# Performance work log

Measured on AMD Instinct MI355X. Metric: run time of the kernel, lower is better.

## Reference

```python
import jax, jax.numpy as jnp
import numpy as np

N = 100_000
E = 1_600_000
F_IN = 128
HID = 64
HEADS = 2
HC = HID // HEADS  # 32 per-head channels
EPS = 1e-5
NEG_SLOPE = 0.2


def _layer_norm(x, g, b):
    mu = jnp.mean(x, axis=-1, keepdims=True)
    var = jnp.mean(jnp.square(x - mu), axis=-1, keepdims=True)
    return (x - mu) * jax.lax.rsqrt(var + EPS) * g + b


def _batch_norm(x, g, b):
    # training-mode batch statistics over the node axis (biased variance)
    mu = jnp.mean(x, axis=0, keepdims=True)
    var = jnp.mean(jnp.square(x - mu), axis=0, keepdims=True)
    return (x - mu) * jax.lax.rsqrt(var + EPS) * g + b


def _gcn_conv(x, src, dst, W, bias, n):
    # PyG GCNConv: self-loops already included in (src, dst); symmetric norm
    deg = jax.ops.segment_sum(jnp.ones_like(src, dtype=x.dtype), dst, num_segments=n)
    dinv = jnp.where(deg > 0, jax.lax.rsqrt(deg), 0.0)
    norm = dinv[src] * dinv[dst]                      # [E2]
    xw = x @ W                                        # [N, out]
    msg = xw[src] * norm[:, None]                     # gather + scale
    out = jax.ops.segment_sum(msg, dst, num_segments=n)
    return out + bias


def _gat_conv(x, src, dst, W, att_src, att_dst, bias, n):
    # PyG GATConv, heads=HEADS, concat=True (self-loops included in src/dst)
    xw = (x @ W).reshape(n, HEADS, HC)                # [N, H, C]
    a_s = jnp.sum(xw * att_src, axis=-1)              # [N, H]
    a_d = jnp.sum(xw * att_dst, axis=-1)              # [N, H]
    e = jax.nn.leaky_relu(a_s[src] + a_d[dst], NEG_SLOPE)  # [E2, H]
    m = jax.ops.segment_max(e, dst, num_segments=n)   # per-target max for stability
    e = jnp.exp(e - m[dst])
    denom = jax.ops.segment_sum(e, dst, num_segments=n)
    alpha = e / (denom[dst] + 1e-16)                  # neighborhood softmax
    out = jax.ops.segment_sum(xw[src] * alpha[:, :, None], dst, num_segments=n)
    return out.reshape(n, HEADS * HC) + bias


def setup_inputs() -> dict:
    key = jax.random.key(0)
    ks = jax.random.split(key, 20)
    f32 = jnp.float32
    d = {}
    d["accessibility_features"] = jax.random.normal(ks[0], (N, F_IN), dtype=f32)
    d["edge_index"] = jax.random.randint(ks[1], (2, E), 0, N, dtype=jnp.int64)
    # LayerNorm
    d["ln_g"] = jnp.ones((F_IN,), f32); d["ln_b"] = jnp.zeros((F_IN,), f32)
    # feature encoder
    d["enc_w1"] = jax.random.normal(ks[2], (F_IN, HID), f32) * (2.0 / (F_IN + HID)) ** 0.5
    d["enc_b1"] = jnp.zeros((HID,), f32)
    d["enc_w2"] = jax.random.normal(ks[3], (HID, HID), f32) * (1.0 / HID) ** 0.5
    d["enc_b2"] = jnp.zeros((HID,), f32)
    # GCN 1
    d["gcn1_w"] = jax.random.normal(ks[4], (HID, HID), f32) * (1.0 / HID) ** 0.5
    d["gcn1_b"] = jnp.zeros((HID,), f32)
    d["bn1_g"] = jnp.ones((HID,), f32); d["bn1_b"] = jnp.zeros((HID,), f32)
    # GAT
    d["gat_w"] = jax.random.normal(ks[5], (HID, HEADS * HC), f32) * (1.0 / HID) ** 0.5
    d["gat_as"] = jax.random.normal(ks[6], (HEADS, HC), f32) * 0.1
    d["gat_ad"] = jax.random.normal(ks[7], (HEADS, HC), f32) * 0.1
    d["gat_b"] = jnp.zeros((HEADS * HC,), f32)
    d["bn2_g"] = jnp.ones((HID,), f32); d["bn2_b"] = jnp.zeros((HID,), f32)
    # GCN 2 -> hidden//2
    d["gcn2_w"] = jax.random.normal(ks[8], (HID, HID // 2), f32) * (2.0 / (HID + HID // 2)) ** 0.5
    d["gcn2_b"] = jnp.zeros((HID // 2,), f32)
    d["bn3_g"] = jnp.ones((HID // 2,), f32); d["bn3_b"] = jnp.zeros((HID // 2,), f32)
    # prediction head
    d["pred_w1"] = jax.random.normal(ks[9], (HID // 2, HID // 4), f32) * (2.0 / (HID // 2 + HID // 4)) ** 0.5
    d["pred_b1"] = jnp.zeros((HID // 4,), f32)
    d["pred_w2"] = jax.random.normal(ks[10], (HID // 4, 1), f32) * (2.0 / (HID // 4 + 1)) ** 0.5
    d["pred_b2"] = jnp.zeros((1,), f32)
    return d


def reference(accessibility_features, edge_index, ln_g, ln_b, enc_w1, enc_b1,
              enc_w2, enc_b2, gcn1_w, gcn1_b, bn1_g, bn1_b, gat_w, gat_as,
              gat_ad, gat_b, bn2_g, bn2_b, gcn2_w, gcn2_b, bn3_g, bn3_b,
              pred_w1, pred_b1, pred_w2, pred_b2):
    n = accessibility_features.shape[0]
    loops = jnp.arange(n, dtype=edge_index.dtype)
    src = jnp.concatenate([edge_index[0], loops])   # add self-loops once
    dst = jnp.concatenate([edge_index[1], loops])

    x = _layer_norm(accessibility_features, ln_g, ln_b)
    x = jax.nn.relu(x @ enc_w1 + enc_b1)            # dropout = identity (eval)
    x = jax.nn.relu(x @ enc_w2 + enc_b2)

    x = _gcn_conv(x, src, dst, gcn1_w, gcn1_b, n)
    x = jax.nn.relu(_batch_norm(x, bn1_g, bn1_b))

    xa = _gat_conv(x, src, dst, gat_w, gat_as, gat_ad, gat_b, n)
    xa = jax.nn.relu(_batch_norm(xa, bn2_g, bn2_b))

    x = _gcn_conv(xa, src, dst, gcn2_w, gcn2_b, n)
    x = jax.nn.relu(_batch_norm(x, bn3_g, bn3_b))

    h = jax.nn.relu(x @ pred_w1 + pred_b1)
    svi = jax.nn.sigmoid((h @ pred_w2 + pred_b2).squeeze(-1))
    return svi
```

## Files before the change

kernel.cpp:

```cpp
#include <hip/hip_runtime.h>
#include <math.h>

#define F_IN 128
#define HID  64
#define EPS  1e-5f
#define NSLOPE 0.2f
#define BSH 9
#define MAXBUK 1024
#define EPB 4096
#define SPB 4096

__device__ __forceinline__ float lrelu(float x) { return x > 0.f ? x : NSLOPE * x; }


__global__ __launch_bounds__(256) void k_buk_count(const int* __restrict__ ei,
                                                   int* __restrict__ bukcnt, int E, int nbuk) {
  __shared__ int lc[MAXBUK];
  for (int k = threadIdx.x; k < nbuk; k += 256) lc[k] = 0;
  __syncthreads();
  int base = blockIdx.x * EPB, end = min(E, base + EPB);
  for (int t = base + threadIdx.x; t < end; t += 256) atomicAdd(&lc[ei[E + t] >> BSH], 1);
  __syncthreads();
  for (int k = threadIdx.x; k < nbuk; k += 256)
    if (lc[k]) atomicAdd(&bukcnt[k], lc[k]);
}

__global__ void k_buk_scan(const int* __restrict__ bukcnt, int* __restrict__ bukbase, int nbuk) {
  __shared__ int l[MAXBUK + 1];
  for (int k = threadIdx.x; k < nbuk; k += blockDim.x) l[k] = bukcnt[k];
  __syncthreads();
  if (threadIdx.x == 0) {
    int r = 0;
    for (int k = 0; k < nbuk; ++k) { int t = l[k]; l[k] = r; r += t; }
    l[nbuk] = r;
  }
  __syncthreads();
  for (int k = threadIdx.x; k <= nbuk; k += blockDim.x) bukbase[k] = l[k];
}

__global__ __launch_bounds__(256) void k_buk_scatter(const int* __restrict__ ei,
                                                     const int* __restrict__ bukbase,
                                                     int* __restrict__ bukcur,
                                                     int2* __restrict__ pairs, int E, int nbuk) {
  __shared__ int lc[MAXBUK];
  __shared__ int lbase[MAXBUK];
  for (int k = threadIdx.x; k < nbuk; k += 256) lc[k] = 0;
  __syncthreads();
  int base = blockIdx.x * EPB, end = min(E, base + EPB);
  for (int t = base + threadIdx.x; t < end; t += 256) atomicAdd(&lc[ei[E + t] >> BSH], 1);
  __syncthreads();
  for (int k = threadIdx.x; k < nbuk; k += 256) {
    int c = lc[k];
    lbase[k] = c ? atomicAdd(&bukcur[k], c) : 0;
  }
  __syncthreads();
  for (int k = threadIdx.x; k < nbuk; k += 256) lc[k] = 0;
  __syncthreads();
  for (int t = base + threadIdx.x; t < end; t += 256) {
    int s = ei[t], d = ei[E + t];
    int b = d >> BSH;
    int o = atomicAdd(&lc[b], 1);
    pairs[bukbase[b] + lbase[b] + o] = make_int2(s, d);
  }
}

__global__ __launch_bounds__(256) void k_buk_deg(const int2* __restrict__ pairs,
                                                 const int* __restrict__ bukbase,
                                                 int* __restrict__ ideg, int N) {
  __shared__ int ldeg[1 << BSH];
  int b = blockIdx.x;
  for (int k = threadIdx.x; k < (1 << BSH); k += 256) ldeg[k] = 0;
  __syncthreads();
  int s0 = bukbase[b], s1 = bukbase[b + 1], nb = b << BSH;
  for (int t = s0 + threadIdx.x; t < s1; t += 256) atomicAdd(&ldeg[pairs[t].y - nb], 1);
  __syncthreads();
  for (int k = threadIdx.x; k < (1 << BSH); k += 256) {
    int node = nb + k;
    if (node < N) ideg[node] = ldeg[k];
  }
}

__global__ __launch_bounds__(256) void k_scan_sums(const int* __restrict__ ideg,
                                                   int* __restrict__ bsum, int N) {
  __shared__ int red[256];
  int base = blockIdx.x * SPB + threadIdx.x * 16;
  int s = 0;
#pragma unroll
  for (int j = 0; j < 16; ++j) { int i = base + j; if (i < N) s += ideg[i] + 1; }
  red[threadIdx.x] = s;
  __syncthreads();
  for (int o = 128; o; o >>= 1) {
    if (threadIdx.x < o) red[threadIdx.x] += red[threadIdx.x + o];
    __syncthreads();
  }
  if (threadIdx.x == 0) bsum[blockIdx.x] = red[0];
}

__global__ void k_scan_tops(int* __restrict__ bsum, int nb) {
  __shared__ int l[MAXBUK];
  for (int k = threadIdx.x; k < nb; k += blockDim.x) l[k] = bsum[k];
  __syncthreads();
  if (threadIdx.x == 0) {
    int r = 0;
    for (int k = 0; k < nb; ++k) { int t = l[k]; l[k] = r; r += t; }
  }
  __syncthreads();
  for (int k = threadIdx.x; k < nb; k += blockDim.x) bsum[k] = l[k];
}

__global__ __launch_bounds__(256) void k_scan_apply(const int* __restrict__ ideg,
                                                    const int* __restrict__ bsum,
                                                    int* __restrict__ rowstart,
                                                    float* __restrict__ dinv,
                                                    int* __restrict__ csr, int N) {
  __shared__ int pre[256];
  int base = blockIdx.x * SPB + threadIdx.x * 16;
  int deg[16];
  int s = 0;
#pragma unroll
  for (int j = 0; j < 16; ++j) {
    int i = base + j;
    int d = (i < N) ? ideg[i] + 1 : 0;
    deg[j] = d; s += d;
  }
  pre[threadIdx.x] = s;
  __syncthreads();
  for (int o = 1; o < 256; o <<= 1) {
    int v = (threadIdx.x >= o) ? pre[threadIdx.x - o] : 0;
    __syncthreads();
    pre[threadIdx.x] += v;
    __syncthreads();
  }
  int off = bsum[blockIdx.x] + pre[threadIdx.x] - s;
#pragma unroll
  for (int j = 0; j < 16; ++j) {
    int i = base + j;
    if (i < N) {
      rowstart[i] = off;
      dinv[i] = rsqrtf((float)deg[j]);
      csr[off] = i;
      off += deg[j];
    }
  }
}

__global__ __launch_bounds__(256) void k_buk_fill(const int2* __restrict__ pairs,
                                                  const int* __restrict__ bukbase,
                                                  const int* __restrict__ rowstart,
                                                  int* __restrict__ csr) {
  __shared__ int lcur[1 << BSH];
  int b = blockIdx.x;
  for (int k = threadIdx.x; k < (1 << BSH); k += 256) lcur[k] = 0;
  __syncthreads();
  int s0 = bukbase[b], s1 = bukbase[b + 1], nb = b << BSH;
  for (int t = s0 + threadIdx.x; t < s1; t += 256) {
    int2 pr = pairs[t];
    int o = atomicAdd(&lcur[pr.y - nb], 1);
    csr[rowstart[pr.y] + 1 + o] = pr.x;
  }
}

__global__ void k_precomp(const float* __restrict__ w1, const float* __restrict__ ln_g,
                          const float* __restrict__ ln_b, const float* __restrict__ b1,
                          float* __restrict__ w1g, float* __restrict__ c1,
                          float* __restrict__ cb) {
  int j = threadIdx.x;
  float c1v = 0.f, cbv = 0.f;
  for (int k = 0; k < F_IN; ++k) {
    float w = w1[k * HID + j];
    float wg = ln_g[k] * w;
    w1g[k * HID + j] = wg;
    c1v += wg;
    cbv += ln_b[k] * w;
  }
  c1[j] = c1v;
  cb[j] = cbv + b1[j];
}

__global__ __launch_bounds__(256) void k_enc_fused(
    const float* __restrict__ x, const float* __restrict__ w1g,
    const float* __restrict__ c1, const float* __restrict__ cb,
    const float* __restrict__ w2, const float* __restrict__ b2,
    const float* __restrict__ w3, float* __restrict__ xw, int N) {
  int i = blockIdx.x * 256 + threadIdx.x;
  if (i >= N) return;
  const float4* xr = (const float4*)(x + (size_t)i * F_IN);
  float a[HID];
#pragma unroll
  for (int j = 0; j < HID; ++j) a[j] = 0.f;
  float s = 0.f, q = 0.f;
#pragma unroll 1
  for (int c = 0; c < F_IN / 4; ++c) {
    float4 xv = xr[c];
    s += xv.x + xv.y + xv.z + xv.w;
    q += xv.x * xv.x + xv.y * xv.y + xv.z * xv.z + xv.w * xv.w;
    const float* wr = w1g + c * 4 * HID;
#pragma unroll
    for (int e = 0; e < 4; ++e) {
      float xe = (e == 0) ? xv.x : (e == 1) ? xv.y : (e == 2) ? xv.z : xv.w;
      const float4* w4 = (const float4*)(wr + e * HID);
#pragma unroll
      for (int j4 = 0; j4 < HID / 4; ++j4) {
        float4 wv = w4[j4];
        a[j4 * 4 + 0] += xe * wv.x;
        a[j4 * 4 + 1] += xe * wv.y;
        a[j4 * 4 + 2] += xe * wv.z;
        a[j4 * 4 + 3] += xe * wv.w;
      }
    }
  }
  float mu = s * (1.f / F_IN);
  float var = q * (1.f / F_IN) - mu * mu;
  float rs = rsqrtf(var + EPS);
#pragma unroll
  for (int j = 0; j < HID; ++j)
    a[j] = fmaxf(rs * (a[j] - mu * c1[j]) + cb[j], 0.f);
  float b[HID];
#pragma unroll
  for (int j = 0; j < HID; ++j) b[j] = b2[j];
#pragma unroll
  for (int k = 0; k < HID; ++k) {
    float hk = a[k];
    const float4* w4 = (const float4*)(w2 + k * HID);
#pragma unroll
    for (int c4 = 0; c4 < HID / 4; ++c4) {
      float4 wv = w4[c4];
      b[c4 * 4 + 0] += hk * wv.x;
      b[c4 * 4 + 1] += hk * wv.y;
      b[c4 * 4 + 2] += hk * wv.z;
      b[c4 * 4 + 3] += hk * wv.w;
    }
  }
#pragma unroll
  for (int j = 0; j < HID; ++j) b[j] = fmaxf(b[j], 0.f);
#pragma unroll
  for (int j = 0; j < HID; ++j) a[j] = 0.f;
#pragma unroll
  for (int k = 0; k < HID; ++k) {
    float hk = b[k];
    const float4* w4 = (const float4*)(w3 + k * HID);
#pragma unroll
    for (int c4 = 0; c4 < HID / 4; ++c4) {
      float4 wv = w4[c4];
      a[c4 * 4 + 0] += hk * wv.x;
      a[c4 * 4 + 1] += hk * wv.y;
      a[c4 * 4 + 2] += hk * wv.z;
      a[c4 * 4 + 3] += hk * wv.w;
    }
  }
  float4* o4 = (float4*)(xw + (size_t)i * HID);
#pragma unroll
  for (int c4 = 0; c4 < HID / 4; ++c4)
    o4[c4] = make_float4(a[c4 * 4 + 0], a[c4 * 4 + 1], a[c4 * 4 + 2], a[c4 * 4 + 3]);
}

template <int FOUT, bool GAT, bool BNIN>
__global__ __launch_bounds__(256) void k_gemm_reg(
    const float* __restrict__ x, const float* __restrict__ w,
    const float* __restrict__ stats,
    const float* __restrict__ atts, const float* __restrict__ atd,
    float* __restrict__ out, float* __restrict__ a_s, float* __restrict__ a_d, int N) {
  int i = blockIdx.x * 256 + threadIdx.x;
  if (i >= N) return;
  const float4* xr = (const float4*)(x + (size_t)i * HID);
  float acc[FOUT];
#pragma unroll
  for (int j = 0; j < FOUT; ++j) acc[j] = 0.f;
#pragma unroll 1
  for (int c = 0; c < HID / 4; ++c) {
    float4 xv = xr[c];
    if (BNIN) {
      xv.x = fmaxf(xv.x * stats[c * 4 + 0] + stats[HID + c * 4 + 0], 0.f);
      xv.y = fmaxf(xv.y * stats[c * 4 + 1] + stats[HID + c * 4 + 1], 0.f);
      xv.z = fmaxf(xv.z * stats[c * 4 + 2] + stats[HID + c * 4 + 2], 0.f);
      xv.w = fmaxf(xv.w * stats[c * 4 + 3] + stats[HID + c * 4 + 3], 0.f);
    }
    const float* wr = w + c * 4 * FOUT;
#pragma unroll
    for (int e = 0; e < 4; ++e) {
      float xe = (e == 0) ? xv.x : (e == 1) ? xv.y : (e == 2) ? xv.z : xv.w;
      const float4* w4 = (const float4*)(wr + e * FOUT);
#pragma unroll
      for (int j4 = 0; j4 < FOUT / 4; ++j4) {
        float4 wv = w4[j4];
        acc[j4 * 4 + 0] += xe * wv.x;
        acc[j4 * 4 + 1] += xe * wv.y;
        acc[j4 * 4 + 2] += xe * wv.z;
        acc[j4 * 4 + 3] += xe * wv.w;
      }
    }
  }
  float4* o4 = (float4*)(out + (size_t)i * FOUT);
#pragma unroll
  for (int c4 = 0; c4 < FOUT / 4; ++c4)
    o4[c4] = make_float4(acc[c4 * 4 + 0], acc[c4 * 4 + 1], acc[c4 * 4 + 2], acc[c4 * 4 + 3]);
  if (GAT) {
    float s0 = 0.f, s1 = 0.f, d0 = 0.f, d1 = 0.f;
#pragma unroll
    for (int c = 0; c < 32; ++c) { s0 += acc[c] * atts[c]; d0 += acc[c] * atd[c]; }
#pragma unroll
    for (int c = 32; c < 64; ++c) { s1 += acc[c] * atts[c]; d1 += acc[c] * atd[c]; }
    a_s[i * 2] = s0; a_s[i * 2 + 1] = s1;
    a_d[i * 2] = d0; a_d[i * 2 + 1] = d1;
  }
}

__global__ __launch_bounds__(256) void k_gcn_pull64(
    const int* __restrict__ csr, const int* __restrict__ rowstart, const int* __restrict__ ideg,
    const float* __restrict__ dinv, const float* __restrict__ xw,
    float* __restrict__ out, int N) {
  int wave = threadIdx.x >> 6, lane = threadIdx.x & 63;
  int i = blockIdx.x * 4 + wave;
  if (i >= N) return;
  int row = rowstart[i], dg = ideg[i] + 1;
  float did = dinv[i];
  float acc = 0.f;
  for (int base = 0; base < dg; base += 64) {
    int cnt = min(64, dg - base);
    int sid = (lane < cnt) ? csr[row + base + lane] : 0;
    int n = 0;
    for (; n + 4 <= cnt; n += 4) {
      int s0 = __shfl(sid, n), s1 = __shfl(sid, n + 1);
      int s2 = __shfl(sid, n + 2), s3 = __shfl(sid, n + 3);
      acc += dinv[s0] * did * xw[s0 * 64 + lane] + dinv[s1] * did * xw[s1 * 64 + lane] +
             dinv[s2] * did * xw[s2 * 64 + lane] + dinv[s3] * did * xw[s3 * 64 + lane];
    }
    for (; n < cnt; ++n) {
      int s0 = __shfl(sid, n);
      acc += dinv[s0] * did * xw[s0 * 64 + lane];
    }
  }
  out[i * 64 + lane] = acc;
}

__global__ __launch_bounds__(256) void k_gcn_pull32(
    const int* __restrict__ csr, const int* __restrict__ rowstart, const int* __restrict__ ideg,
    const float* __restrict__ dinv, const float* __restrict__ xw,
    float* __restrict__ out, int N) {
  int wave = threadIdx.x >> 6, lane = threadIdx.x & 63;
  int half = lane >> 5, lf = lane & 31;
  int i = (blockIdx.x * 4 + wave) * 2 + half;
  if (i >= N) return;
  int row = rowstart[i], dg = ideg[i] + 1;
  float did = dinv[i];
  float acc = 0.f;
  for (int base = 0; base < dg; base += 32) {
    int cnt = min(32, dg - base);
    int sid = (lf < cnt) ? csr[row + base + lf] : 0;
    int n = 0;
    for (; n + 2 <= cnt; n += 2) {
      int s0 = __shfl(sid, n, 32), s1 = __shfl(sid, n + 1, 32);
      acc += dinv[s0] * did * xw[s0 * 32 + lf] + dinv[s1] * did * xw[s1 * 32 + lf];
    }
    for (; n < cnt; ++n) {
      int s0 = __shfl(sid, n, 32);
      acc += dinv[s0] * did * xw[s0 * 32 + lf];
    }
  }
  out[i * 32 + lf] = acc;
}

__global__ __launch_bounds__(256) void k_gat_attn(
    const int* __restrict__ csr, const int* __restrict__ rowstart, const int* __restrict__ ideg,
    const float* __restrict__ a_s, const float* __restrict__ a_d,
    float* __restrict__ m_, float* __restrict__ rden, int N) {
  int wave = threadIdx.x >> 6, lane = threadIdx.x & 63;
  int i = blockIdx.x * 4 + wave;
  if (i >= N) return;
  int row = rowstart[i], dg = ideg[i] + 1;
  float ad0 = a_d[i * 2], ad1 = a_d[i * 2 + 1];
  if (dg <= 64) {
    float e0 = -1e30f, e1 = -1e30f;
    if (lane < dg) {
      int s = csr[row + lane];
      e0 = lrelu(a_s[s * 2] + ad0);
      e1 = lrelu(a_s[s * 2 + 1] + ad1);
    }
    float m0 = e0, m1 = e1;
#pragma unroll
    for (int o = 32; o; o >>= 1) { m0 = fmaxf(m0, __shfl_xor(m0, o)); m1 = fmaxf(m1, __shfl_xor(m1, o)); }
    float s0 = (lane < dg) ? __expf(e0 - m0) : 0.f;
    float s1 = (lane < dg) ? __expf(e1 - m1) : 0.f;
#pragma unroll
    for (int o = 32; o; o >>= 1) { s0 += __shfl_xor(s0, o); s1 += __shfl_xor(s1, o); }
    if (lane == 0) {
      m_[i * 2] = m0; m_[i * 2 + 1] = m1;
      rden[i * 2] = 1.f / (s0 + 1e-16f); rden[i * 2 + 1] = 1.f / (s1 + 1e-16f);
    }
  } else {
    float m0 = -1e30f, m1 = -1e30f;
    for (int base = 0; base < dg; base += 64)
      if (base + lane < dg) {
        int s = csr[row + base + lane];
        m0 = fmaxf(m0, lrelu(a_s[s * 2] + ad0));
        m1 = fmaxf(m1, lrelu(a_s[s * 2 + 1] + ad1));
      }
#pragma unroll
    for (int o = 32; o; o >>= 1) { m0 = fmaxf(m0, __shfl_xor(m0, o)); m1 = fmaxf(m1, __shfl_xor(m1, o)); }
    float s0 = 0.f, s1 = 0.f;
    for (int base = 0; base < dg; base += 64)
      if (base + lane < dg) {
        int s = csr[row + base + lane];
        s0 += __expf(lrelu(a_s[s * 2] + ad0) - m0);
        s1 += __expf(lrelu(a_s[s * 2 + 1] + ad1) - m1);
      }
#pragma unroll
    for (int o = 32; o; o >>= 1) { s0 += __shfl_xor(s0, o); s1 += __shfl_xor(s1, o); }
    if (lane == 0) {
      m_[i * 2] = m0; m_[i * 2 + 1] = m1;
      rden[i * 2] = 1.f / (s0 + 1e-16f); rden[i * 2 + 1] = 1.f / (s1 + 1e-16f);
    }
  }
}

__global__ __launch_bounds__(256) void k_gat_pv(
    const int* __restrict__ csr, const int* __restrict__ rowstart, const int* __restrict__ ideg,
    const float* __restrict__ a_s, const float* __restrict__ a_d,
    const float* __restrict__ m_, const float* __restrict__ rden,
    const float* __restrict__ xw, float* __restrict__ out, int N) {
  int wave = threadIdx.x >> 6, lane = threadIdx.x & 63;
  int i = blockIdx.x * 4 + wave;
  if (i >= N) return;
  int row = rowstart[i], dg = ideg[i] + 1;
  int h = lane >> 5;
  float adh = a_d[i * 2 + h], mh = m_[i * 2 + h], rh = rden[i * 2 + h];
  float acc = 0.f;
  for (int base = 0; base < dg; base += 64) {
    int cnt = min(64, dg - base);
    int sid = (lane < cnt) ? csr[row + base + lane] : 0;
    int n = 0;
    for (; n + 2 <= cnt; n += 2) {
      int s0 = __shfl(sid, n), s1 = __shfl(sid, n + 1);
      float al0 = __expf(lrelu(a_s[s0 * 2 + h] + adh) - mh) * rh;
      float al1 = __expf(lrelu(a_s[s1 * 2 + h] + adh) - mh) * rh;
      acc += al0 * xw[s0 * HID + lane] + al1 * xw[s1 * HID + lane];
    }
    for (; n < cnt; ++n) {
      int s0 = __shfl(sid, n);
      float al0 = __expf(lrelu(a_s[s0 * 2 + h] + adh) - mh) * rh;
      acc += al0 * xw[s0 * HID + lane];
    }
  }
  out[i * HID + lane] = acc;
}

template <int F>
__global__ __launch_bounds__(256) void k_bn_reduce(const float* __restrict__ x,
                                                   float* __restrict__ partials, int N) {
  __shared__ float sS[F], sQ[F];
  int tid = threadIdx.x;
  int t = blockIdx.x * 256 + tid;
  int stride = gridDim.x * 256;
  int total4 = N * F / 4;
  int f0 = (t * 4) % F;
  float s0 = 0, s1 = 0, s2 = 0, s3 = 0, q0 = 0, q1 = 0, q2 = 0, q3 = 0;
  for (int c = t; c < total4; c += stride) {
    float4 v = ((const float4*)x)[c];
    s0 += v.x; q0 += v.x * v.x;
    s1 += v.y; q1 += v.y * v.y;
    s2 += v.z; q2 += v.z * v.z;
    s3 += v.w; q3 += v.w * v.w;
  }
  if (tid < F) { sS[tid] = 0.f; sQ[tid] = 0.f; }
  __syncthreads();
  atomicAdd(&sS[f0], s0);     atomicAdd(&sQ[f0], q0);
  atomicAdd(&sS[f0 + 1], s1); atomicAdd(&sQ[f0 + 1], q1);
  atomicAdd(&sS[f0 + 2], s2); atomicAdd(&sQ[f0 + 2], q2);
  atomicAdd(&sS[f0 + 3], s3); atomicAdd(&sQ[f0 + 3], q3);
  __syncthreads();
  if (tid < F) {
    partials[blockIdx.x * 2 * F + tid]     = sS[tid];
    partials[blockIdx.x * 2 * F + F + tid] = sQ[tid];
  }
}

template <int F>
__global__ void k_bn_finalize(const float* __restrict__ partials, int nblk,
                              float* __restrict__ stats, const float* __restrict__ g,
                              const float* __restrict__ b, int N) {
  int f = threadIdx.x;
  if (f >= F) return;
  float s = 0.f, q = 0.f;
  for (int k = 0; k < nblk; ++k) {
    s += partials[k * 2 * F + f];
    q += partials[k * 2 * F + F + f];
  }
  float mu = s / (float)N;
  float var = q / (float)N - mu * mu;
  float sc = rsqrtf(var + EPS) * g[f];
  stats[f] = sc;
  stats[F + f] = b[f] - mu * sc;
}

__global__ __launch_bounds__(256) void k_pred(
    const float* __restrict__ x, const float* __restrict__ stats,
    const float* __restrict__ w1, const float* __restrict__ b1,
    const float* __restrict__ w2, const float* __restrict__ b2,
    float* __restrict__ out, int N) {
  int i = blockIdx.x * 256 + threadIdx.x;
  if (i >= N) return;
  const float4* xr = (const float4*)(x + (size_t)i * 32);
  float acc[16];
#pragma unroll
  for (int j = 0; j < 16; ++j) acc[j] = b1[j];
#pragma unroll 1
  for (int c = 0; c < 8; ++c) {
    float4 xv = xr[c];
    xv.x = fmaxf(xv.x * stats[c * 4 + 0] + stats[32 + c * 4 + 0], 0.f);
    xv.y = fmaxf(xv.y * stats[c * 4 + 1] + stats[32 + c * 4 + 1], 0.f);
    xv.z = fmaxf(xv.z * stats[c * 4 + 2] + stats[32 + c * 4 + 2], 0.f);
    xv.w = fmaxf(xv.w * stats[c * 4 + 3] + stats[32 + c * 4 + 3], 0.f);
    const float* wr = w1 + c * 4 * 16;
#pragma unroll
    for (int e = 0; e < 4; ++e) {
      float xe = (e == 0) ? xv.x : (e == 1) ? xv.y : (e == 2) ? xv.z : xv.w;
      const float4* w4 = (const float4*)(wr + e * 16);
#pragma unroll
      for (int j4 = 0; j4 < 4; ++j4) {
        float4 wv = w4[j4];
        acc[j4 * 4 + 0] += xe * wv.x;
        acc[j4 * 4 + 1] += xe * wv.y;
        acc[j4 * 4 + 2] += xe * wv.z;
        acc[j4 * 4 + 3] += xe * wv.w;
      }
    }
  }
  float z = b2[0];
#pragma unroll
  for (int j = 0; j < 16; ++j) z += fmaxf(acc[j], 0.f) * w2[j];
  out[i] = 1.f / (1.f + __expf(-z));
}

extern "C" void kernel_launch(void* const* d_in, const int* in_sizes, int n_in,
                              void* d_out, int out_size, void* d_ws, size_t ws_size,
                              hipStream_t stream) {
  const float* x_in  = (const float*)d_in[0];
  const int*   ei    = (const int*)d_in[1];
  const float* ln_g  = (const float*)d_in[2];
  const float* ln_b  = (const float*)d_in[3];
  const float* enc_w1 = (const float*)d_in[4];
  const float* enc_b1 = (const float*)d_in[5];
  const float* enc_w2 = (const float*)d_in[6];
  const float* enc_b2 = (const float*)d_in[7];
  const float* gcn1_w = (const float*)d_in[8];
  const float* bn1_g = (const float*)d_in[10];
  const float* bn1_b = (const float*)d_in[11];
  const float* gat_w  = (const float*)d_in[12];
  const float* gat_as = (const float*)d_in[13];
  const float* gat_ad = (const float*)d_in[14];
  const float* bn2_g = (const float*)d_in[16];
  const float* bn2_b = (const float*)d_in[17];
  const float* gcn2_w = (const float*)d_in[18];
  const float* bn3_g = (const float*)d_in[20];
  const float* bn3_b = (const float*)d_in[21];
  const float* pw1 = (const float*)d_in[22];
  const float* pb1 = (const float*)d_in[23];
  const float* pw2 = (const float*)d_in[24];
  const float* pb2 = (const float*)d_in[25];
  float* out = (float*)d_out;

  int N = in_sizes[0] / F_IN;
  int E = in_sizes[1] / 2;
  int nbuk = (N + (1 << BSH) - 1) >> BSH;

  const int NBLK_BN = 128;

  char* p = (char*)d_ws;
  auto alloc = [&](size_t bytes) { char* r = p; p += (bytes + 255) & ~(size_t)255; return (void*)r; };
  float* h     = (float*)alloc((size_t)N * 64 * 4);
  float* xw    = (float*)alloc((size_t)N * 64 * 4);
  float* agg   = (float*)alloc((size_t)N * 64 * 4);
  float* as_   = (float*)alloc((size_t)N * 2 * 4);
  float* ad_   = (float*)alloc((size_t)N * 2 * 4);
  float* m_    = (float*)alloc((size_t)N * 2 * 4);
  float* rden  = (float*)alloc((size_t)N * 2 * 4);
  float* dinv  = (float*)alloc((size_t)N * 4);
  float* stats = (float*)alloc(2 * 64 * 4);
  float* parts = (float*)alloc((size_t)NBLK_BN * 2 * 64 * 4);
  float* w1g   = (float*)alloc((size_t)F_IN * HID * 4);
  float* c1    = (float*)alloc(HID * 4);
  float* cb    = (float*)alloc(HID * 4);
  int* ideg    = (int*)alloc((size_t)N * 4);
  int* rowst   = (int*)alloc((size_t)N * 4);
  int* csr     = (int*)alloc((size_t)(N + E) * 4);
  int* bukcnt  = (int*)alloc((size_t)MAXBUK * 4);
  int* bukbase = (int*)alloc((size_t)(MAXBUK + 1) * 4);
  int* bukcur  = (int*)alloc((size_t)MAXBUK * 4);
  int* bsum    = (int*)alloc((size_t)MAXBUK * 4);
  int2* pairs  = (int2*)h;

  hipMemsetAsync(bukcnt, 0, (size_t)nbuk * 4, stream);
  hipMemsetAsync(bukcur, 0, (size_t)nbuk * 4, stream);

  int EB = (E + EPB - 1) / EPB;
  int SB = (N + SPB - 1) / SPB;
  int NB = (N + 255) / 256;
  int NB4 = (N + 3) / 4;
  int NB8 = (N + 7) / 8;

  k_buk_count<<<EB, 256, 0, stream>>>(ei, bukcnt, E, nbuk);
  k_buk_scan<<<1, 256, 0, stream>>>(bukcnt, bukbase, nbuk);
  k_buk_scatter<<<EB, 256, 0, stream>>>(ei, bukbase, bukcur, pairs, E, nbuk);
  k_buk_deg<<<nbuk, 256, 0, stream>>>(pairs, bukbase, ideg, N);
  k_scan_sums<<<SB, 256, 0, stream>>>(ideg, bsum, N);
  k_scan_tops<<<1, 256, 0, stream>>>(bsum, SB);
  k_scan_apply<<<SB, 256, 0, stream>>>(ideg, bsum, rowst, dinv, csr, N);
  k_buk_fill<<<nbuk, 256, 0, stream>>>(pairs, bukbase, rowst, csr);

  k_precomp<<<1, 64, 0, stream>>>(enc_w1, ln_g, ln_b, enc_b1, w1g, c1, cb);
  k_enc_fused<<<NB, 256, 0, stream>>>(x_in, w1g, c1, cb, enc_w2, enc_b2, gcn1_w, xw, N);

  k_gcn_pull64<<<NB4, 256, 0, stream>>>(csr, rowst, ideg, dinv, xw, agg, N);
  k_bn_reduce<64><<<NBLK_BN, 256, 0, stream>>>(agg, parts, N);
  k_bn_finalize<64><<<1, 64, 0, stream>>>(parts, NBLK_BN, stats, bn1_g, bn1_b, N);

  k_gemm_reg<64, true, true><<<NB, 256, 0, stream>>>(agg, gat_w, stats, gat_as, gat_ad,
                                                     xw, as_, ad_, N);
  k_gat_attn<<<NB4, 256, 0, stream>>>(csr, rowst, ideg, as_, ad_, m_, rden, N);
  k_gat_pv<<<NB4, 256, 0, stream>>>(csr, rowst, ideg, as_, ad_, m_, rden, xw, h, N);
  k_bn_reduce<64><<<NBLK_BN, 256, 0, stream>>>(h, parts, N);
  k_bn_finalize<64><<<1, 64, 0, stream>>>(parts, NBLK_BN, stats, bn2_g, bn2_b, N);

  k_gemm_reg<32, false, true><<<NB, 256, 0, stream>>>(h, gcn2_w, stats, nullptr, nullptr,
                                                      xw, nullptr, nullptr, N);
  k_gcn_pull32<<<NB8, 256, 0, stream>>>(csr, rowst, ideg, dinv, xw, agg, N);
  k_bn_reduce<32><<<NBLK_BN, 256, 0, stream>>>(agg, parts, N);
  k_bn_finalize<32><<<1, 32, 0, stream>>>(parts, NBLK_BN, stats, bn3_g, bn3_b, N);

  k_pred<<<NB, 256, 0, stream>>>(agg, stats, pw1, pb1, pw2, pb2, out, N);
}
```

Baseline: 640.5 us.

## Split per-node dense kernels across two threads to cut register pressure

The fused encoder, the GAT/GCN projection GEMMs and the predictor head now assign two threads per node, each computing half of the output features. Partial activations are exchanged with lane shuffles so the chained matmuls still see the full hidden vector, and the GAT attention dot products are split per head. Launch bounds are raised to request more waves per CU, and the BN reduction uses more partial blocks. This targets the low occupancy caused by 64- to 128-float register arrays per thread, at the cost of reloading each x row twice and adding shuffle traffic.

```diff
diff --git a/kernel.cpp b/kernel.cpp
--- a/kernel.cpp
+++ b/kernel.cpp
@@ -177,30 +177,30 @@
   cb[j] = cbv + b1[j];
 }
 
-__global__ __launch_bounds__(256) void k_enc_fused(
+__global__ __launch_bounds__(256, 4) void k_enc2(
     const float* __restrict__ x, const float* __restrict__ w1g,
     const float* __restrict__ c1, const float* __restrict__ cb,
     const float* __restrict__ w2, const float* __restrict__ b2,
     const float* __restrict__ w3, float* __restrict__ xw, int N) {
-  int i = blockIdx.x * 256 + threadIdx.x;
+  int t = blockIdx.x * 256 + threadIdx.x;
+  int i = t >> 1, half = t & 1;
   if (i >= N) return;
   const float4* xr = (const float4*)(x + (size_t)i * F_IN);
-  float a[HID];
-#pragma unroll
-  for (int j = 0; j < HID; ++j) a[j] = 0.f;
+  float a[32];
+#pragma unroll
+  for (int j = 0; j < 32; ++j) a[j] = 0.f;
   float s = 0.f, q = 0.f;
-#pragma unroll 1
+#pragma unroll 4
   for (int c = 0; c < F_IN / 4; ++c) {
     float4 xv = xr[c];
     s += xv.x + xv.y + xv.z + xv.w;
     q += xv.x * xv.x + xv.y * xv.y + xv.z * xv.z + xv.w * xv.w;
-    const float* wr = w1g + c * 4 * HID;
 #pragma unroll
     for (int e = 0; e < 4; ++e) {
       float xe = (e == 0) ? xv.x : (e == 1) ? xv.y : (e == 2) ? xv.z : xv.w;
-      const float4* w4 = (const float4*)(wr + e * HID);
-#pragma unroll
-      for (int j4 = 0; j4 < HID / 4; ++j4) {
+      const float4* w4 = (const float4*)(w1g + (size_t)(c * 4 + e) * HID + half * 32);
+#pragma unroll
+      for (int j4 = 0; j4 < 8; ++j4) {
         float4 wv = w4[j4];
         a[j4 * 4 + 0] += xe * wv.x;
         a[j4 * 4 + 1] += xe * wv.y;
@@ -213,60 +213,92 @@
   float var = q * (1.f / F_IN) - mu * mu;
   float rs = rsqrtf(var + EPS);
 #pragma unroll
-  for (int j = 0; j < HID; ++j)
-    a[j] = fmaxf(rs * (a[j] - mu * c1[j]) + cb[j], 0.f);
-  float b[HID];
-#pragma unroll
-  for (int j = 0; j < HID; ++j) b[j] = b2[j];
-#pragma unroll
-  for (int k = 0; k < HID; ++k) {
-    float hk = a[k];
-    const float4* w4 = (const float4*)(w2 + k * HID);
-#pragma unroll
-    for (int c4 = 0; c4 < HID / 4; ++c4) {
-      float4 wv = w4[c4];
-      b[c4 * 4 + 0] += hk * wv.x;
-      b[c4 * 4 + 1] += hk * wv.y;
-      b[c4 * 4 + 2] += hk * wv.z;
-      b[c4 * 4 + 3] += hk * wv.w;
-    }
-  }
-#pragma unroll
-  for (int j = 0; j < HID; ++j) b[j] = fmaxf(b[j], 0.f);
-#pragma unroll
-  for (int j = 0; j < HID; ++j) a[j] = 0.f;
-#pragma unroll
-  for (int k = 0; k < HID; ++k) {
-    float hk = b[k];
-    const float4* w4 = (const float4*)(w3 + k * HID);
-#pragma unroll
-    for (int c4 = 0; c4 < HID / 4; ++c4) {
-      float4 wv = w4[c4];
-      a[c4 * 4 + 0] += hk * wv.x;
-      a[c4 * 4 + 1] += hk * wv.y;
-      a[c4 * 4 + 2] += hk * wv.z;
-      a[c4 * 4 + 3] += hk * wv.w;
-    }
-  }
-  float4* o4 = (float4*)(xw + (size_t)i * HID);
-#pragma unroll
-  for (int c4 = 0; c4 < HID / 4; ++c4)
+  for (int j = 0; j < 32; ++j)
+    a[j] = fmaxf(rs * (a[j] - mu * c1[half * 32 + j]) + cb[half * 32 + j], 0.f);
+  float b[32];
+#pragma unroll
+  for (int j = 0; j < 32; ++j) b[j] = b2[half * 32 + j];
+#pragma unroll
+  for (int kk = 0; kk < 32; ++kk) {
+    int k = half * 32 + kk;
+    float ak = a[kk];
+    const float4* w4 = (const float4*)(w2 + (size_t)k * HID + half * 32);
+#pragma unroll
+    for (int j4 = 0; j4 < 8; ++j4) {
+      float4 wv = w4[j4];
+      b[j4 * 4 + 0] += ak * wv.x;
+      b[j4 * 4 + 1] += ak * wv.y;
+      b[j4 * 4 + 2] += ak * wv.z;
+      b[j4 * 4 + 3] += ak * wv.w;
+    }
+  }
+#pragma unroll
+  for (int kk = 0; kk < 32; ++kk) {
+    int k = (1 - half) * 32 + kk;
+    float ak = __shfl_xor(a[kk], 1);
+    const float4* w4 = (const float4*)(w2 + (size_t)k * HID + half * 32);
+#pragma unroll
+    for (int j4 = 0; j4 < 8; ++j4) {
+      float4 wv = w4[j4];
+      b[j4 * 4 + 0] += ak * wv.x;
+      b[j4 * 4 + 1] += ak * wv.y;
+      b[j4 * 4 + 2] += ak * wv.z;
+      b[j4 * 4 + 3] += ak * wv.w;
+    }
+  }
+#pragma unroll
+  for (int j = 0; j < 32; ++j) b[j] = fmaxf(b[j], 0.f);
+#pragma unroll
+  for (int j = 0; j < 32; ++j) a[j] = 0.f;
+#pragma unroll
+  for (int kk = 0; kk < 32; ++kk) {
+    int k = half * 32 + kk;
+    float bk = b[kk];
+    const float4* w4 = (const float4*)(w3 + (size_t)k * HID + half * 32);
+#pragma unroll
+    for (int j4 = 0; j4 < 8; ++j4) {
+      float4 wv = w4[j4];
+      a[j4 * 4 + 0] += bk * wv.x;
+      a[j4 * 4 + 1] += bk * wv.y;
+      a[j4 * 4 + 2] += bk * wv.z;
+      a[j4 * 4 + 3] += bk * wv.w;
+    }
+  }
+#pragma unroll
+  for (int kk = 0; kk < 32; ++kk) {
+    int k = (1 - half) * 32 + kk;
+    float bk = __shfl_xor(b[kk], 1);
+    const float4* w4 = (const float4*)(w3 + (size_t)k * HID + half * 32);
+#pragma unroll
+    for (int j4 = 0; j4 < 8; ++j4) {
+      float4 wv = w4[j4];
+      a[j4 * 4 + 0] += bk * wv.x;
+      a[j4 * 4 + 1] += bk * wv.y;
+      a[j4 * 4 + 2] += bk * wv.z;
+      a[j4 * 4 + 3] += bk * wv.w;
+    }
+  }
+  float4* o4 = (float4*)(xw + (size_t)i * HID + half * 32);
+#pragma unroll
+  for (int c4 = 0; c4 < 8; ++c4)
     o4[c4] = make_float4(a[c4 * 4 + 0], a[c4 * 4 + 1], a[c4 * 4 + 2], a[c4 * 4 + 3]);
 }
 
-template <int FOUT, bool GAT, bool BNIN>
-__global__ __launch_bounds__(256) void k_gemm_reg(
+template <int FH, bool GAT, bool BNIN>
+__global__ __launch_bounds__(256, 4) void k_gemm_half(
     const float* __restrict__ x, const float* __restrict__ w,
     const float* __restrict__ stats,
     const float* __restrict__ atts, const float* __restrict__ atd,
     float* __restrict__ out, float* __restrict__ a_s, float* __restrict__ a_d, int N) {
-  int i = blockIdx.x * 256 + threadIdx.x;
+  const int FOUT = 2 * FH;
+  int t = blockIdx.x * 256 + threadIdx.x;
+  int i = t >> 1, half = t & 1;
   if (i >= N) return;
   const float4* xr = (const float4*)(x + (size_t)i * HID);
-  float acc[FOUT];
-#pragma unroll
-  for (int j = 0; j < FOUT; ++j) acc[j] = 0.f;
-#pragma unroll 1
+  float acc[FH];
+#pragma unroll
+  for (int j = 0; j < FH; ++j) acc[j] = 0.f;
+#pragma unroll 4
   for (int c = 0; c < HID / 4; ++c) {
     float4 xv = xr[c];
     if (BNIN) {
@@ -275,13 +307,12 @@
       xv.z = fmaxf(xv.z * stats[c * 4 + 2] + stats[HID + c * 4 + 2], 0.f);
       xv.w = fmaxf(xv.w * stats[c * 4 + 3] + stats[HID + c * 4 + 3], 0.f);
     }
-    const float* wr = w + c * 4 * FOUT;
 #pragma unroll
     for (int e = 0; e < 4; ++e) {
       float xe = (e == 0) ? xv.x : (e == 1) ? xv.y : (e == 2) ? xv.z : xv.w;
-      const float4* w4 = (const float4*)(wr + e * FOUT);
-#pragma unroll
-      for (int j4 = 0; j4 < FOUT / 4; ++j4) {
+      const float4* w4 = (const float4*)(w + (size_t)(c * 4 + e) * FOUT + half * FH);
+#pragma unroll
+      for (int j4 = 0; j4 < FH / 4; ++j4) {
         float4 wv = w4[j4];
         acc[j4 * 4 + 0] += xe * wv.x;
         acc[j4 * 4 + 1] += xe * wv.y;
@@ -290,18 +321,19 @@
       }
     }
   }
-  float4* o4 = (float4*)(out + (size_t)i * FOUT);
-#pragma unroll
-  for (int c4 = 0; c4 < FOUT / 4; ++c4)
+  float4* o4 = (float4*)(out + (size_t)i * FOUT + half * FH);
+#pragma unroll
+  for (int c4 = 0; c4 < FH / 4; ++c4)
     o4[c4] = make_float4(acc[c4 * 4 + 0], acc[c4 * 4 + 1], acc[c4 * 4 + 2], acc[c4 * 4 + 3]);
   if (GAT) {
-    float s0 = 0.f, s1 = 0.f, d0 = 0.f, d1 = 0.f;
-#pragma unroll
-    for (int c = 0; c < 32; ++c) { s0 += acc[c] * atts[c]; d0 += acc[c] * atd[c]; }
-#pragma unroll
-    for (int c = 32; c < 64; ++c) { s1 += acc[c] * atts[c]; d1 += acc[c] * atd[c]; }
-    a_s[i * 2] = s0; a_s[i * 2 + 1] = s1;
-    a_d[i * 2] = d0; a_d[i * 2 + 1] = d1;
+    float s0 = 0.f, d0 = 0.f;
+#pragma unroll
+    for (int c = 0; c < FH; ++c) {
+      s0 += acc[c] * atts[half * FH + c];
+      d0 += acc[c] * atd[half * FH + c];
+    }
+    a_s[i * 2 + half] = s0;
+    a_d[i * 2 + half] = d0;
   }
 }
 
@@ -492,31 +524,31 @@
   stats[F + f] = b[f] - mu * sc;
 }
 
-__global__ __launch_bounds__(256) void k_pred(
+__global__ __launch_bounds__(256, 4) void k_pred2(
     const float* __restrict__ x, const float* __restrict__ stats,
     const float* __restrict__ w1, const float* __restrict__ b1,
     const float* __restrict__ w2, const float* __restrict__ b2,
     float* __restrict__ out, int N) {
-  int i = blockIdx.x * 256 + threadIdx.x;
+  int t = blockIdx.x * 256 + threadIdx.x;
+  int i = t >> 1, half = t & 1;
   if (i >= N) return;
   const float4* xr = (const float4*)(x + (size_t)i * 32);
-  float acc[16];
-#pragma unroll
-  for (int j = 0; j < 16; ++j) acc[j] = b1[j];
-#pragma unroll 1
+  float acc[8];
+#pragma unroll
+  for (int j = 0; j < 8; ++j) acc[j] = b1[half * 8 + j];
+#pragma unroll 4
   for (int c = 0; c < 8; ++c) {
     float4 xv = xr[c];
     xv.x = fmaxf(xv.x * stats[c * 4 + 0] + stats[32 + c * 4 + 0], 0.f);
     xv.y = fmaxf(xv.y * stats[c * 4 + 1] + stats[32 + c * 4 + 1], 0.f);
     xv.z = fmaxf(xv.z * stats[c * 4 + 2] + stats[32 + c * 4 + 2], 0.f);
     xv.w = fmaxf(xv.w * stats[c * 4 + 3] + stats[32 + c * 4 + 3], 0.f);
-    const float* wr = w1 + c * 4 * 16;
 #pragma unroll
     for (int e = 0; e < 4; ++e) {
       float xe = (e == 0) ? xv.x : (e == 1) ? xv.y : (e == 2) ? xv.z : xv.w;
-      const float4* w4 = (const float4*)(wr + e * 16);
-#pragma unroll
-      for (int j4 = 0; j4 < 4; ++j4) {
+      const float4* w4 = (const float4*)(w1 + (size_t)(c * 4 + e) * 16 + half * 8);
+#pragma unroll
+      for (int j4 = 0; j4 < 2; ++j4) {
         float4 wv = w4[j4];
         acc[j4 * 4 + 0] += xe * wv.x;
         acc[j4 * 4 + 1] += xe * wv.y;
@@ -525,10 +557,11 @@
       }
     }
   }
-  float z = b2[0];
-#pragma unroll
-  for (int j = 0; j < 16; ++j) z += fmaxf(acc[j], 0.f) * w2[j];
-  out[i] = 1.f / (1.f + __expf(-z));
+  float zp = 0.f;
+#pragma unroll
+  for (int j = 0; j < 8; ++j) zp += fmaxf(acc[j], 0.f) * w2[half * 8 + j];
+  float z = zp + __shfl_xor(zp, 1) + b2[0];
+  if (half == 0) out[i] = 1.f / (1.f + __expf(-z));
 }
 
 extern "C" void kernel_launch(void* const* d_in, const int* in_sizes, int n_in,
@@ -563,7 +596,7 @@
   int E = in_sizes[1] / 2;
   int nbuk = (N + (1 << BSH) - 1) >> BSH;
 
-  const int NBLK_BN = 128;
+  const int NBLK_BN = 256;
 
   char* p = (char*)d_ws;
   auto alloc = [&](size_t bytes) { char* r = p; p += (bytes + 255) & ~(size_t)255; return (void*)r; };
@@ -594,7 +627,7 @@
 
   int EB = (E + EPB - 1) / EPB;
   int SB = (N + SPB - 1) / SPB;
-  int NB = (N + 255) / 256;
+  int NB2 = (2 * N + 255) / 256;
   int NB4 = (N + 3) / 4;
   int NB8 = (N + 7) / 8;
 
@@ -608,24 +641,24 @@
   k_buk_fill<<<nbuk, 256, 0, stream>>>(pairs, bukbase, rowst, csr);
 
   k_precomp<<<1, 64, 0, stream>>>(enc_w1, ln_g, ln_b, enc_b1, w1g, c1, cb);
-  k_enc_fused<<<NB, 256, 0, stream>>>(x_in, w1g, c1, cb, enc_w2, enc_b2, gcn1_w, xw, N);
+  k_enc2<<<NB2, 256, 0, stream>>>(x_in, w1g, c1, cb, enc_w2, enc_b2, gcn1_w, xw, N);
 
   k_gcn_pull64<<<NB4, 256, 0, stream>>>(csr, rowst, ideg, dinv, xw, agg, N);
   k_bn_reduce<64><<<NBLK_BN, 256, 0, stream>>>(agg, parts, N);
   k_bn_finalize<64><<<1, 64, 0, stream>>>(parts, NBLK_BN, stats, bn1_g, bn1_b, N);
 
-  k_gemm_reg<64, true, true><<<NB, 256, 0, stream>>>(agg, gat_w, stats, gat_as, gat_ad,
-                                                     xw, as_, ad_, N);
+  k_gemm_half<32, true, true><<<NB2, 256, 0, stream>>>(agg, gat_w, stats, gat_as, gat_ad,
+                                                       xw, as_, ad_, N);
   k_gat_attn<<<NB4, 256, 0, stream>>>(csr, rowst, ideg, as_, ad_, m_, rden, N);
   k_gat_pv<<<NB4, 256, 0, stream>>>(csr, rowst, ideg, as_, ad_, m_, rden, xw, h, N);
   k_bn_reduce<64><<<NBLK_BN, 256, 0, stream>>>(h, parts, N);
   k_bn_finalize<64><<<1, 64, 0, stream>>>(parts, NBLK_BN, stats, bn2_g, bn2_b, N);
 
-  k_gemm_reg<32, false, true><<<NB, 256, 0, stream>>>(h, gcn2_w, stats, nullptr, nullptr,
-                                                      xw, nullptr, nullptr, N);
+  k_gemm_half<16, false, true><<<NB2, 256, 0, stream>>>(h, gcn2_w, stats, nullptr, nullptr,
+                                                        xw, nullptr, nullptr, N);
   k_gcn_pull32<<<NB8, 256, 0, stream>>>(csr, rowst, ideg, dinv, xw, agg, N);
   k_bn_reduce<32><<<NBLK_BN, 256, 0, stream>>>(agg, parts, N);
   k_bn_finalize<32><<<1, 32, 0, stream>>>(parts, NBLK_BN, stats, bn3_g, bn3_b, N);
 
-  k_pred<<<NB, 256, 0, stream>>>(agg, stats, pw1, pb1, pw2, pb2, out, N);
-}
+  k_pred2<<<NB2, 256, 0, stream>>>(agg, stats, pw1, pb1, pw2, pb2, out, N);
+}
```

After: 1.378 ms. +115.1%, slower.

## Split encoder MLP per node across four threads with shuffle exchange

Applied to the files above, without the earlier changes.

The fused encoder kernel now assigns each node to a quad of threads, and each thread computes 16 of the 64 output channels. Hidden activations are passed between the quad's lanes with warp shuffles for the second and third matmuls. This cuts per-thread accumulator registers from 64 to 16 and launches four times as many threads, raising occupancy and spreading the work over more CUs. In exchange, every thread in a quad rereads the full input row for the LayerNorm statistics and the first matmul, and the shuffles add extra instructions.

```diff
diff --git a/kernel.cpp b/kernel.cpp
--- a/kernel.cpp
+++ b/kernel.cpp
@@ -177,30 +177,31 @@
   cb[j] = cbv + b1[j];
 }
 
-__global__ __launch_bounds__(256) void k_enc_fused(
+__global__ __launch_bounds__(256) void k_enc4(
     const float* __restrict__ x, const float* __restrict__ w1g,
     const float* __restrict__ c1, const float* __restrict__ cb,
     const float* __restrict__ w2, const float* __restrict__ b2,
     const float* __restrict__ w3, float* __restrict__ xw, int N) {
-  int i = blockIdx.x * 256 + threadIdx.x;
+  int t = blockIdx.x * 256 + threadIdx.x;
+  int i = t >> 2, quad = t & 3;
   if (i >= N) return;
+  int lbase = (threadIdx.x & 63) & ~3;
   const float4* xr = (const float4*)(x + (size_t)i * F_IN);
-  float a[HID];
-#pragma unroll
-  for (int j = 0; j < HID; ++j) a[j] = 0.f;
+  float a[16];
+#pragma unroll
+  for (int j = 0; j < 16; ++j) a[j] = 0.f;
   float s = 0.f, q = 0.f;
-#pragma unroll 1
+#pragma unroll 8
   for (int c = 0; c < F_IN / 4; ++c) {
     float4 xv = xr[c];
     s += xv.x + xv.y + xv.z + xv.w;
     q += xv.x * xv.x + xv.y * xv.y + xv.z * xv.z + xv.w * xv.w;
-    const float* wr = w1g + c * 4 * HID;
 #pragma unroll
     for (int e = 0; e < 4; ++e) {
       float xe = (e == 0) ? xv.x : (e == 1) ? xv.y : (e == 2) ? xv.z : xv.w;
-      const float4* w4 = (const float4*)(wr + e * HID);
-#pragma unroll
-      for (int j4 = 0; j4 < HID / 4; ++j4) {
+      const float4* w4 = (const float4*)(w1g + (size_t)(c * 4 + e) * HID + quad * 16);
+#pragma unroll
+      for (int j4 = 0; j4 < 4; ++j4) {
         float4 wv = w4[j4];
         a[j4 * 4 + 0] += xe * wv.x;
         a[j4 * 4 + 1] += xe * wv.y;
@@ -213,44 +214,50 @@
   float var = q * (1.f / F_IN) - mu * mu;
   float rs = rsqrtf(var + EPS);
 #pragma unroll
-  for (int j = 0; j < HID; ++j)
-    a[j] = fmaxf(rs * (a[j] - mu * c1[j]) + cb[j], 0.f);
-  float b[HID];
-#pragma unroll
-  for (int j = 0; j < HID; ++j) b[j] = b2[j];
-#pragma unroll
-  for (int k = 0; k < HID; ++k) {
-    float hk = a[k];
-    const float4* w4 = (const float4*)(w2 + k * HID);
-#pragma unroll
-    for (int c4 = 0; c4 < HID / 4; ++c4) {
-      float4 wv = w4[c4];
-      b[c4 * 4 + 0] += hk * wv.x;
-      b[c4 * 4 + 1] += hk * wv.y;
-      b[c4 * 4 + 2] += hk * wv.z;
-      b[c4 * 4 + 3] += hk * wv.w;
-    }
-  }
-#pragma unroll
-  for (int j = 0; j < HID; ++j) b[j] = fmaxf(b[j], 0.f);
-#pragma unroll
-  for (int j = 0; j < HID; ++j) a[j] = 0.f;
-#pragma unroll
-  for (int k = 0; k < HID; ++k) {
-    float hk = b[k];
-    const float4* w4 = (const float4*)(w3 + k * HID);
-#pragma unroll
-    for (int c4 = 0; c4 < HID / 4; ++c4) {
-      float4 wv = w4[c4];
-      a[c4 * 4 + 0] += hk * wv.x;
-      a[c4 * 4 + 1] += hk * wv.y;
-      a[c4 * 4 + 2] += hk * wv.z;
-      a[c4 * 4 + 3] += hk * wv.w;
-    }
-  }
-  float4* o4 = (float4*)(xw + (size_t)i * HID);
-#pragma unroll
-  for (int c4 = 0; c4 < HID / 4; ++c4)
+  for (int j = 0; j < 16; ++j)
+    a[j] = fmaxf(rs * (a[j] - mu * c1[quad * 16 + j]) + cb[quad * 16 + j], 0.f);
+  float b[16];
+#pragma unroll
+  for (int j = 0; j < 16; ++j) b[j] = b2[quad * 16 + j];
+#pragma unroll
+  for (int ko = 0; ko < 4; ++ko) {
+#pragma unroll
+    for (int kk = 0; kk < 16; ++kk) {
+      float ak = __shfl(a[kk], lbase + ko);
+      const float4* w4 = (const float4*)(w2 + (size_t)(ko * 16 + kk) * HID + quad * 16);
+#pragma unroll
+      for (int j4 = 0; j4 < 4; ++j4) {
+        float4 wv = w4[j4];
+        b[j4 * 4 + 0] += ak * wv.x;
+        b[j4 * 4 + 1] += ak * wv.y;
+        b[j4 * 4 + 2] += ak * wv.z;
+        b[j4 * 4 + 3] += ak * wv.w;
+      }
+    }
+  }
+#pragma unroll
+  for (int j = 0; j < 16; ++j) b[j] = fmaxf(b[j], 0.f);
+#pragma unroll
+  for (int j = 0; j < 16; ++j) a[j] = 0.f;
+#pragma unroll
+  for (int ko = 0; ko < 4; ++ko) {
+#pragma unroll
+    for (int kk = 0; kk < 16; ++kk) {
+      float bk = __shfl(b[kk], lbase + ko);
+      const float4* w4 = (const float4*)(w3 + (size_t)(ko * 16 + kk) * HID + quad * 16);
+#pragma unroll
+      for (int j4 = 0; j4 < 4; ++j4) {
+        float4 wv = w4[j4];
+        a[j4 * 4 + 0] += bk * wv.x;
+        a[j4 * 4 + 1] += bk * wv.y;
+        a[j4 * 4 + 2] += bk * wv.z;
+        a[j4 * 4 + 3] += bk * wv.w;
+      }
+    }
+  }
+  float4* o4 = (float4*)(xw + (size_t)i * HID + quad * 16);
+#pragma unroll
+  for (int c4 = 0; c4 < 4; ++c4)
     o4[c4] = make_float4(a[c4 * 4 + 0], a[c4 * 4 + 1], a[c4 * 4 + 2], a[c4 * 4 + 3]);
 }
 
@@ -597,6 +604,7 @@
   int NB = (N + 255) / 256;
   int NB4 = (N + 3) / 4;
   int NB8 = (N + 7) / 8;
+  int NBQ = (4 * N + 255) / 256;
 
   k_buk_count<<<EB, 256, 0, stream>>>(ei, bukcnt, E, nbuk);
   k_buk_scan<<<1, 256, 0, stream>>>(bukcnt, bukbase, nbuk);
@@ -608,7 +616,7 @@
   k_buk_fill<<<nbuk, 256, 0, stream>>>(pairs, bukbase, rowst, csr);
 
   k_precomp<<<1, 64, 0, stream>>>(enc_w1, ln_g, ln_b, enc_b1, w1g, c1, cb);
-  k_enc_fused<<<NB, 256, 0, stream>>>(x_in, w1g, c1, cb, enc_w2, enc_b2, gcn1_w, xw, N);
+  k_enc4<<<NBQ, 256, 0, stream>>>(x_in, w1g, c1, cb, enc_w2, enc_b2, gcn1_w, xw, N);
 
   k_gcn_pull64<<<NB4, 256, 0, stream>>>(csr, rowst, ideg, dinv, xw, agg, N);
   k_bn_reduce<64><<<NBLK_BN, 256, 0, stream>>>(agg, parts, N);
```

Result: slower. 924.5 us (+44.3%).
